# Kernel optimization log

Measured on AMD Instinct MI355X. Metric: run time of the kernel, lower is better.

The kernel has to match this reference:

```python
import jax, jax.numpy as jnp
import numpy as np

INPUT_DIM = 512
HEAD_NUM = 8
ATT_SIZE = 64
EPS = 1e-5


def layer_norm(x, g, b):
    mu = jnp.mean(x, axis=-1, keepdims=True)
    var = jnp.mean(jnp.square(x - mu), axis=-1, keepdims=True)
    return (x - mu) * jax.lax.rsqrt(var + EPS) * g + b


def setup_inputs() -> dict:
    key = jax.random.key(0)
    ks = jax.random.split(key, 10)
    D, H, A = INPUT_DIM, HEAD_NUM, ATT_SIZE
    HA = H * A
    s = lambda fan_in: 1.0 / np.sqrt(fan_in)
    x = jax.random.normal(ks[0], (32, 6, 256, D), dtype=jnp.float32)
    # Linear weights stored as [in, out] so y = x @ W + b (matches torch x @ W.T)
    Wq = jax.random.uniform(ks[1], (D, HA), jnp.float32, -s(D), s(D))
    bq = jnp.zeros((HA,), jnp.float32)
    Wk = jax.random.uniform(ks[2], (D, HA), jnp.float32, -s(D), s(D))
    bk = jnp.zeros((HA,), jnp.float32)
    Wv = jax.random.uniform(ks[3], (D, HA), jnp.float32, -s(D), s(D))
    bv = jnp.zeros((HA,), jnp.float32)
    Wo = jax.random.uniform(ks[4], (HA, D), jnp.float32, -s(HA), s(HA))
    bo = jnp.zeros((D,), jnp.float32)
    g1 = jnp.ones((D,), jnp.float32)
    b1 = jnp.zeros((D,), jnp.float32)
    Wd = jax.random.uniform(ks[5], (2 * D, D), jnp.float32, -s(2 * D), s(2 * D))
    bd = jnp.zeros((D,), jnp.float32)
    g2 = jnp.ones((D,), jnp.float32)
    b2 = jnp.zeros((D,), jnp.float32)
    return dict(x=x, Wq=Wq, bq=bq, Wk=Wk, bk=bk, Wv=Wv, bv=bv,
                Wo=Wo, bo=bo, g1=g1, b1=b1, Wd=Wd, bd=bd, g2=g2, b2=b2)


def reference(x, Wq, bq, Wk, bk, Wv, bv, Wo, bo, g1, b1, Wd, bd, g2, b2):
    B, M, P, D = x.shape
    H, A = HEAD_NUM, ATT_SIZE
    # QKV projections -> [B, M, H, P, A]
    q = (x @ Wq + bq).reshape(B, M, P, H, A).transpose(0, 1, 3, 2, 4)
    k = (x @ Wk + bk).reshape(B, M, P, H, A).transpose(0, 1, 3, 2, 4)
    v = (x @ Wv + bv).reshape(B, M, P, H, A).transpose(0, 1, 3, 2, 4)
    scores = jnp.einsum('bmhqa,bmhka->bmhqk', q, k) / jnp.sqrt(jnp.float32(A))
    attn = jax.nn.softmax(scores, axis=-1)
    z = jnp.einsum('bmhqk,bmhka->bmhqa', attn, v)
    z = z.transpose(0, 1, 3, 2, 4).reshape(B, M, P, H * A)
    z = jax.nn.relu(x + layer_norm(z @ Wo + bo, g1, b1))
    # patch merge (1/2 downsample)
    if P % 2:  # static shape check, fine under jit
        z = jnp.pad(z, ((0, 0), (0, 0), (0, 1), (0, 0)))
    merged = jnp.concatenate([z[:, :, 0::2, :], z[:, :, 1::2, :]], axis=-1)
    out = jax.nn.relu(layer_norm(merged @ Wd + bd, g2, b2))
    return out
```

## Files before the change

### kernel.cpp

```cpp
#include <hip/hip_runtime.h>
#include <hip/hip_bf16.h>
#include <stdint.h>


typedef __hip_bfloat16 bf16;
typedef __attribute__((ext_vector_type(8))) __bf16 bf16v8;
typedef __attribute__((ext_vector_type(4))) float f32x4;
typedef __attribute__((ext_vector_type(8))) short s16x8;
typedef __attribute__((ext_vector_type(4))) short s16x4;

static __device__ __forceinline__ void gl_lds16(const void* src, void* dst) {
  __builtin_amdgcn_global_load_lds((const __attribute__((address_space(1))) void*)src,
                                   (__attribute__((address_space(3))) void*)dst,
                                   16, 0, 0);
}

static __device__ __forceinline__ unsigned short f2bfu(float f) {
  return __builtin_bit_cast(unsigned short, __float2bfloat16(f));
}
static __device__ __forceinline__ float bfu2f(unsigned short u) {
  return __builtin_bit_cast(float, (unsigned int)u << 16);
}

__global__ __launch_bounds__(256) void conv_x_kernel(const float4* __restrict__ x,
                                                     s16x4* __restrict__ xb, int n4) {
  int stride = gridDim.x * 256;
  for (int i = blockIdx.x * 256 + threadIdx.x; i < n4; i += stride) {
    float4 v = x[i];
    s16x4 o;
    o[0] = (short)f2bfu(v.x); o[1] = (short)f2bfu(v.y);
    o[2] = (short)f2bfu(v.z); o[3] = (short)f2bfu(v.w);
    xb[i] = o;
  }
}

__global__ __launch_bounds__(256) void conv_w_kernel(
    const float* __restrict__ Wq, const float* __restrict__ Wk, const float* __restrict__ Wv,
    const float* __restrict__ Wo, const float* __restrict__ Wd,
    const float* __restrict__ bq, const float* __restrict__ bk, const float* __restrict__ bv,
    bf16* __restrict__ wqkv_t, bf16* __restrict__ wo_t, bf16* __restrict__ wd_t,
    float* __restrict__ bqkv) {
  int o = blockIdx.x * 256 + threadIdx.x;
  if (o < 786432) {
    int j = o >> 9, kk = o & 511;
    const float* W = (j < 512) ? Wq : (j < 1024) ? Wk : Wv;
    wqkv_t[o] = __float2bfloat16(W[kk * 512 + (j & 511)]);
  } else if (o < 1048576) {
    int o2 = o - 786432; int j = o2 >> 9, kk = o2 & 511;
    wo_t[o2] = __float2bfloat16(Wo[kk * 512 + j]);
  } else if (o < 1572864) {
    int o3 = o - 1048576; int j = o3 >> 10, kk = o3 & 1023;
    wd_t[o3] = __float2bfloat16(Wd[kk * 512 + j]);
  } else if (o < 1574400) {
    int o4 = o - 1572864;
    const float* b = (o4 < 512) ? bq : (o4 < 1024) ? bk : bv;
    bqkv[o4] = b[o4 & 511];
  }
}

template<int EPI, int AMODE>
__global__ __launch_bounds__(512, 2) void gemm256(
    const bf16* __restrict__ A, const bf16* __restrict__ Bt,
    const float* __restrict__ bias, int K, int nN,
    bf16* __restrict__ oq, bf16* __restrict__ ok, bf16* __restrict__ ovt,
    bf16* __restrict__ obf) {
  __shared__ __align__(16) char smem[131072];
  const int tid = threadIdx.x;
  const int wave = tid >> 6, lane = tid & 63;
  const int wr = wave >> 2, wc = wave & 3;
  const int lane15 = lane & 15, g = lane >> 4;

  const int cpx = gridDim.x >> 3;
  const int lin = (blockIdx.x & 7) * cpx + (blockIdx.x >> 3);
  const int tileM = (lin / nN) * 256, tileN = (lin % nN) * 256;

  const int rT = tid >> 3;
  const int cT = (tid & 7) ^ (rT & 7);
  const int iters = K >> 7;

  auto stage = [&](int tau, int q) {
    char* dst = smem + ((tau & 1) << 16) + ((q >> 1) << 15) + ((q & 1) << 14) + tid * 16;
    int kpos = tau * 64 + cT * 8;
    if (q < 2) {
      int rowA = tileM + ((q & 1) << 7) + rT;
      if (AMODE == 0) {
        const bf16* s0 = A + (size_t)rowA * K + kpos;
        gl_lds16(s0, dst);
        gl_lds16(s0 + (size_t)64 * K, dst + 8192);
      } else {
#pragma unroll
        for (int j = 0; j < 2; ++j) {
          int mr = rowA + j * 64;
          int bm = mr >> 7, pp = mr & 127;
          const bf16* s = A + (size_t)(bm * 256 + pp * 2 + (kpos >> 9)) * 512 + (kpos & 511);
          gl_lds16(s, dst + j * 8192);
        }
      }
    } else {
      int rowB = tileN + ((q & 1) << 7) + rT;
      const bf16* s0 = Bt + (size_t)rowB * K + kpos;
      gl_lds16(s0, dst);
      gl_lds16(s0 + (size_t)64 * K, dst + 8192);
    }
  };

  f32x4 acc[8][4] = {};
  bf16v8 areg[4][2], breg[2][2];

  stage(0, 0); stage(0, 1); stage(0, 2); stage(0, 3);
  stage(1, 0); stage(1, 1);
  asm volatile("s_waitcnt vmcnt(4)" ::: "memory");
  __builtin_amdgcn_s_barrier();

  for (int it = 0; it < iters; ++it) {
    const bool last = (it == iters - 1);
#pragma unroll
    for (int p = 0; p < 8; ++p) {
      const int buf = p >> 2;
      const int mh = (p >> 1) & 1, nh = p & 1;
      char* Ab = smem + (buf << 16);
      char* Bb = Ab + 32768;
      if (nh == 0) {
#pragma unroll
        for (int f = 0; f < 4; ++f) {
          int row = wr * 128 + (mh * 4 + f) * 16 + lane15;
#pragma unroll
          for (int ks = 0; ks < 2; ++ks)
            areg[f][ks] = *(const bf16v8*)(Ab + row * 128 + (((ks * 4 + g) ^ (row & 7)) << 4));
        }
      }
#pragma unroll
      for (int n = 0; n < 2; ++n) {
        int row = wc * 64 + (nh * 2 + n) * 16 + lane15;
#pragma unroll
        for (int ks = 0; ks < 2; ++ks)
          breg[n][ks] = *(const bf16v8*)(Bb + row * 128 + (((ks * 4 + g) ^ (row & 7)) << 4));
      }
      if (p == 0)      { stage(2 * it + 1, 2); stage(2 * it + 1, 3); }
      else if (p == 3) { if (!last) { stage(2 * it + 2, 0); stage(2 * it + 2, 1); } }
      else if (p == 4) { if (!last) { stage(2 * it + 2, 2); stage(2 * it + 2, 3); } }
      else if (p == 7) { if (!last) { stage(2 * it + 3, 0); stage(2 * it + 3, 1); } }
      __builtin_amdgcn_s_setprio(1);
#pragma unroll
      for (int ks = 0; ks < 2; ++ks)
#pragma unroll
        for (int f = 0; f < 4; ++f)
#pragma unroll
          for (int n = 0; n < 2; ++n)
            acc[mh * 4 + f][nh * 2 + n] = __builtin_amdgcn_mfma_f32_16x16x32_bf16(
                areg[f][ks], breg[n][ks], acc[mh * 4 + f][nh * 2 + n], 0, 0, 0);
      __builtin_amdgcn_s_setprio(0);
      if (p == 2 || p == 6) {
        asm volatile("s_waitcnt lgkmcnt(0)" ::: "memory");
        __builtin_amdgcn_s_barrier();
      } else if (p == 3) {
        if (last) { asm volatile("s_waitcnt vmcnt(0) lgkmcnt(0)" ::: "memory"); }
        else      { asm volatile("s_waitcnt vmcnt(4) lgkmcnt(0)" ::: "memory"); }
        __builtin_amdgcn_s_barrier();
      } else if (p == 7) {
        if (last) { asm volatile("s_waitcnt lgkmcnt(0)" ::: "memory"); }
        else      { asm volatile("s_waitcnt vmcnt(4) lgkmcnt(0)" ::: "memory"); }
        __builtin_amdgcn_s_barrier();
      }
    }
  }

  if (EPI == 0 && tileN >= 1024) {
    const int hh = ((tileN - 1024) >> 6) + wc;
    const int bm = tileM >> 8;
    char* slab = smem + wave * 16384;
#pragma unroll
    for (int fm = 0; fm < 8; ++fm) {
#pragma unroll
      for (int fn = 0; fn < 4; ++fn) {
        int col = tileN + wc * 64 + fn * 16 + lane15;
        float bb = bias[col];
        int a = fn * 16 + lane15;
#pragma unroll
        for (int i = 0; i < 4; ++i) {
          int pl = fm * 16 + g * 4 + i;
          *(bf16*)(slab + a * 256 + ((pl * 2) ^ ((a & 7) << 4))) =
              __float2bfloat16(acc[fm][fn][i] + bb);
        }
      }
    }
    asm volatile("" ::: "memory");
    bf16* vdst = ovt + ((size_t)(bm * 8 + hh) << 14) + wr * 128;
#pragma unroll
    for (int r = 0; r < 16; ++r) {
      int a = r * 4 + (lane >> 4);
      int ps = lane & 15;
      s16x8 vv = *(const s16x8*)(slab + a * 256 + ((ps * 16) ^ ((a & 7) << 4)));
      *(s16x8*)(vdst + a * 256 + ps * 8) = vv;
    }
  } else {
    char* slab = smem + wave * 16384;
#pragma unroll
    for (int fm = 0; fm < 8; ++fm) {
#pragma unroll
      for (int fn = 0; fn < 4; ++fn) {
        int col = tileN + wc * 64 + fn * 16 + lane15;
        float bb = bias[col];
        int lb = (fn * 16 + lane15) * 2;
#pragma unroll
        for (int i = 0; i < 4; ++i) {
          int pl = fm * 16 + g * 4 + i;
          *(bf16*)(slab + pl * 128 + (lb ^ ((((pl >> 2) & 3)) << 5))) =
              __float2bfloat16(acc[fm][fn][i] + bb);
        }
      }
    }
    asm volatile("" ::: "memory");
    bf16* dst; int ldc2;
    if (EPI == 0) {
      int cb = tileN + wc * 64;
      int hh = (cb >> 6) & 7;
      bf16* base = (cb < 512) ? oq : ok;
      dst = base + (((size_t)((tileM >> 8) * 8 + hh)) << 14) + wr * 128 * 64;
      ldc2 = 64;
    } else {
      dst = obf + (size_t)(tileM + wr * 128) * 512 + tileN + wc * 64;
      ldc2 = 512;
    }
#pragma unroll
    for (int r = 0; r < 16; ++r) {
      int s = r * 64 + lane;
      int pl = s >> 3, sl = s & 7;
      s16x8 vv = *(const s16x8*)(slab + pl * 128 + ((sl * 16) ^ ((((pl >> 2) & 3)) << 5)));
      *(s16x8*)(dst + (size_t)pl * ldc2 + sl * 8) = vv;
    }
  }
}

__global__ __launch_bounds__(256) void attn_kernel(const bf16* __restrict__ q,
                                                   const bf16* __restrict__ k,
                                                   const bf16* __restrict__ vt,
                                                   bf16* __restrict__ z) {
  __shared__ __align__(16) char smem[81920];
  const int tid = threadIdx.x, wave = tid >> 6, lane = tid & 63;
  const int lane15 = lane & 15, g = lane >> 4;
  const int qc = blockIdx.x, hh = blockIdx.y, bm = blockIdx.z;
  const int bh = bm * 8 + hh;
  const bf16* kbase = k + ((size_t)bh << 14);
  const bf16* vbase = vt + ((size_t)bh << 14);
  const bf16* qbase = q + ((size_t)bh << 14) + (qc * 64 + wave * 16) * 64;

#pragma unroll
  for (int i = 0; i < 8; ++i) {
    int s = i * 256 + tid;
    int kr = s >> 3, ksp = s & 7;
    gl_lds16(kbase + kr * 64 + (ksp ^ (kr & 7)) * 8, smem + s * 16);
    int ar = s >> 5, asp = s & 31;
    gl_lds16(vbase + ar * 256 + (asp ^ (ar & 7)) * 8, smem + 32768 + s * 16);
  }
  bf16v8 qf[2];
#pragma unroll
  for (int kk = 0; kk < 2; ++kk)
    qf[kk] = *(const bf16v8*)(qbase + lane15 * 64 + kk * 32 + g * 8);
  __syncthreads();

  f32x4 sacc[16] = {};
#pragma unroll
  for (int tl = 0; tl < 16; ++tl) {
    int key = tl * 16 + lane15;
    int rb = key * 128, swk = (key & 7) << 4;
#pragma unroll
    for (int kk = 0; kk < 2; ++kk) {
      bf16v8 kf = *(const bf16v8*)(smem + rb + (((kk * 4 + g) * 16) ^ swk));
      sacc[tl] = __builtin_amdgcn_mfma_f32_16x16x32_bf16(qf[kk], kf, sacc[tl], 0, 0, 0);
    }
  }

  float mx[4], sm[4], rcp[4];
#pragma unroll
  for (int i = 0; i < 4; ++i) mx[i] = sacc[0][i];
#pragma unroll
  for (int tl = 1; tl < 16; ++tl)
#pragma unroll
    for (int i = 0; i < 4; ++i) mx[i] = fmaxf(mx[i], sacc[tl][i]);
#pragma unroll
  for (int i = 0; i < 4; ++i) {
    mx[i] = fmaxf(mx[i], __shfl_xor(mx[i], 1));
    mx[i] = fmaxf(mx[i], __shfl_xor(mx[i], 2));
    mx[i] = fmaxf(mx[i], __shfl_xor(mx[i], 4));
    mx[i] = fmaxf(mx[i], __shfl_xor(mx[i], 8));
    sm[i] = 0.f;
  }
#pragma unroll
  for (int tl = 0; tl < 16; ++tl)
#pragma unroll
    for (int i = 0; i < 4; ++i) {
      float e = __expf((sacc[tl][i] - mx[i]) * 0.125f);
      sacc[tl][i] = e; sm[i] += e;
    }
#pragma unroll
  for (int i = 0; i < 4; ++i) {
    sm[i] += __shfl_xor(sm[i], 1);
    sm[i] += __shfl_xor(sm[i], 2);
    sm[i] += __shfl_xor(sm[i], 4);
    sm[i] += __shfl_xor(sm[i], 8);
    rcp[i] = 1.0f / sm[i];
  }

  char* pbase = smem + 65536 + wave * 4096;
  f32x4 oacc[4] = {};
#pragma unroll
  for (int h2 = 0; h2 < 2; ++h2) {
#pragma unroll
    for (int t8 = 0; t8 < 8; ++t8) {
      int tl = h2 * 8 + t8;
#pragma unroll
      for (int i = 0; i < 4; ++i) {
        int r = g * 4 + i;
        int c2 = t8 * 16 + lane15;
        *(bf16*)(pbase + r * 256 + ((c2 * 2) ^ ((r & 7) << 4))) =
            __float2bfloat16(sacc[tl][i] * rcp[i]);
      }
    }
    asm volatile("" ::: "memory");
#pragma unroll
    for (int k2 = 0; k2 < 4; ++k2) {
      int ks = h2 * 4 + k2;
      bf16v8 pf = *(const bf16v8*)(pbase + lane15 * 256 +
                                   ((k2 * 64 + g * 16) ^ ((lane15 & 7) << 4)));
#pragma unroll
      for (int at = 0; at < 4; ++at) {
        int a = at * 16 + lane15;
        bf16v8 vf = *(const bf16v8*)(smem + 32768 + a * 512 +
                                     ((ks * 64 + g * 16) ^ ((a & 7) << 4)));
        oacc[at] = __builtin_amdgcn_mfma_f32_16x16x32_bf16(pf, vf, oacc[at], 0, 0, 0);
      }
    }
    asm volatile("" ::: "memory");
  }

  int trow = bm * 256 + qc * 64 + wave * 16;
#pragma unroll
  for (int at = 0; at < 4; ++at)
#pragma unroll
    for (int i = 0; i < 4; ++i)
      z[(size_t)(trow + g * 4 + i) * 512 + hh * 64 + at * 16 + lane15] =
          __float2bfloat16(oacc[at][i]);
}

static __device__ __forceinline__ float wredsum(float v) {
  v += __shfl_xor(v, 1);  v += __shfl_xor(v, 2);  v += __shfl_xor(v, 4);
  v += __shfl_xor(v, 8);  v += __shfl_xor(v, 16); v += __shfl_xor(v, 32);
  return v;
}

__global__ __launch_bounds__(256) void ln_res_kernel(const bf16* __restrict__ y1,
                                                     const float* __restrict__ x,
                                                     const float* __restrict__ g1,
                                                     const float* __restrict__ b1,
                                                     bf16* __restrict__ z2) {
  const int wave = threadIdx.x >> 6, lane = threadIdx.x & 63;
  const int row = blockIdx.x * 4 + wave;
  const size_t base = (size_t)row * 512 + lane * 8;
  s16x8 yv = *(const s16x8*)(y1 + base);
  float f[8];
#pragma unroll
  for (int j = 0; j < 8; ++j) f[j] = bfu2f((unsigned short)yv[j]);
  float s = 0.f, s2 = 0.f;
#pragma unroll
  for (int j = 0; j < 8; ++j) { s += f[j]; s2 += f[j] * f[j]; }
  s = wredsum(s); s2 = wredsum(s2);
  float mu = s * (1.f / 512.f);
  float var = s2 * (1.f / 512.f) - mu * mu;
  float rs = rsqrtf(var + 1e-5f);
  float4 x0 = *(const float4*)(x + base);
  float4 x1 = *(const float4*)(x + base + 4);
  float xa[8] = {x0.x, x0.y, x0.z, x0.w, x1.x, x1.y, x1.z, x1.w};
  float ga[8], ba[8];
#pragma unroll
  for (int j = 0; j < 8; ++j) { ga[j] = g1[lane * 8 + j]; ba[j] = b1[lane * 8 + j]; }
  s16x8 ov;
#pragma unroll
  for (int j = 0; j < 8; ++j) {
    float v = xa[j] + (f[j] - mu) * rs * ga[j] + ba[j];
    ov[j] = (short)f2bfu(fmaxf(v, 0.f));
  }
  *(s16x8*)(z2 + base) = ov;
}

__global__ __launch_bounds__(256) void ln_out_kernel(const bf16* __restrict__ y2,
                                                     const float* __restrict__ g2,
                                                     const float* __restrict__ b2,
                                                     float* __restrict__ out) {
  const int wave = threadIdx.x >> 6, lane = threadIdx.x & 63;
  const int row = blockIdx.x * 4 + wave;
  const size_t base = (size_t)row * 512 + lane * 8;
  s16x8 yv = *(const s16x8*)(y2 + base);
  float f[8];
#pragma unroll
  for (int j = 0; j < 8; ++j) f[j] = bfu2f((unsigned short)yv[j]);
  float s = 0.f, s2 = 0.f;
#pragma unroll
  for (int j = 0; j < 8; ++j) { s += f[j]; s2 += f[j] * f[j]; }
  s = wredsum(s); s2 = wredsum(s2);
  float mu = s * (1.f / 512.f);
  float var = s2 * (1.f / 512.f) - mu * mu;
  float rs = rsqrtf(var + 1e-5f);
  float o[8];
#pragma unroll
  for (int j = 0; j < 8; ++j)
    o[j] = fmaxf((f[j] - mu) * rs * g2[lane * 8 + j] + b2[lane * 8 + j], 0.f);
  float4 w0 = {o[0], o[1], o[2], o[3]};
  float4 w1 = {o[4], o[5], o[6], o[7]};
  *(float4*)(out + base) = w0;
  *(float4*)(out + base + 4) = w1;
}

extern "C" void kernel_launch(void* const* d_in, const int* in_sizes, int n_in,
                              void* d_out, int out_size, void* d_ws, size_t ws_size,
                              hipStream_t stream) {
  const float* x  = (const float*)d_in[0];
  const float* Wq = (const float*)d_in[1];
  const float* bq = (const float*)d_in[2];
  const float* Wk = (const float*)d_in[3];
  const float* bk = (const float*)d_in[4];
  const float* Wv = (const float*)d_in[5];
  const float* bv = (const float*)d_in[6];
  const float* Wo = (const float*)d_in[7];
  const float* bo = (const float*)d_in[8];
  const float* g1 = (const float*)d_in[9];
  const float* b1 = (const float*)d_in[10];
  const float* Wd = (const float*)d_in[11];
  const float* bd = (const float*)d_in[12];
  const float* g2 = (const float*)d_in[13];
  const float* b2 = (const float*)d_in[14];

  char* ws = (char*)d_ws;
  const size_t SEG = 50331648;
  bf16*  xb   = (bf16*)(ws);
  bf16*  qb   = (bf16*)(ws + SEG);
  bf16*  kb   = (bf16*)(ws + 2 * SEG);
  bf16*  vtb  = (bf16*)(ws + 3 * SEG);
  bf16*  wqkv = (bf16*)(ws + 4 * SEG);
  bf16*  wot  = (bf16*)(ws + 4 * SEG + 1572864);
  bf16*  wdt  = (bf16*)(ws + 4 * SEG + 2097152);
  float* bqkv = (float*)(ws + 4 * SEG + 3145728);
  bf16*  zb   = xb;
  bf16*  y1   = qb;
  bf16*  z2   = kb;
  bf16*  y2   = vtb;

  conv_x_kernel<<<4096, 256, 0, stream>>>((const float4*)x, (s16x4*)xb, 25165824 / 4);
  conv_w_kernel<<<6150, 256, 0, stream>>>(Wq, Wk, Wv, Wo, Wd, bq, bk, bv,
                                          wqkv, wot, wdt, bqkv);
  gemm256<0, 0><<<1152, 512, 0, stream>>>(xb, wqkv, bqkv, 512, 6,
                                          qb, kb, vtb, nullptr);
  attn_kernel<<<dim3(4, 8, 192), 256, 0, stream>>>(qb, kb, vtb, zb);
  gemm256<1, 0><<<384, 512, 0, stream>>>(zb, wot, bo, 512, 2,
                                         nullptr, nullptr, nullptr, y1);
  ln_res_kernel<<<12288, 256, 0, stream>>>(y1, x, g1, b1, z2);
  gemm256<1, 1><<<192, 512, 0, stream>>>(z2, wdt, bd, 1024, 2,
                                         nullptr, nullptr, nullptr, y2);
  ln_out_kernel<<<6144, 256, 0, stream>>>(y2, g2, b2, (float*)d_out);
}
```

Baseline: 332.5 us.

## Shrink GEMM tiles from 256x256 to 128x128 with 4-wave blocks

Replaces the 256x256, 512-thread GEMM with a 128x128, 256-thread version that uses half the LDS, and adapts the staging, fragment loads and epilogues to the new tile. All three GEMM launches now use 4x more blocks, which improves wave fill across the CUs, especially for the small out-projection and downsample GEMMs that had only 384 and 192 blocks. The trade-off is lower arithmetic intensity per tile and more global/L2 traffic for operand reloads. It also caches B fragments across phases to avoid re-reading LDS.

```diff
diff --git a/kernel.cpp b/kernel.cpp
--- a/kernel.cpp
+++ b/kernel.cpp
@@ -59,53 +59,51 @@
 }
 
 template<int EPI, int AMODE>
-__global__ __launch_bounds__(512, 2) void gemm256(
+__global__ __launch_bounds__(256, 2) void gemm128(
     const bf16* __restrict__ A, const bf16* __restrict__ Bt,
     const float* __restrict__ bias, int K, int nN,
     bf16* __restrict__ oq, bf16* __restrict__ ok, bf16* __restrict__ ovt,
     bf16* __restrict__ obf) {
-  __shared__ __align__(16) char smem[131072];
+  __shared__ __align__(16) char smem[65536];
   const int tid = threadIdx.x;
   const int wave = tid >> 6, lane = tid & 63;
-  const int wr = wave >> 2, wc = wave & 3;
+  const int wr = wave >> 1, wc = wave & 1;
   const int lane15 = lane & 15, g = lane >> 4;
 
   const int cpx = gridDim.x >> 3;
   const int lin = (blockIdx.x & 7) * cpx + (blockIdx.x >> 3);
-  const int tileM = (lin / nN) * 256, tileN = (lin % nN) * 256;
-
-  const int rT = tid >> 3;
-  const int cT = (tid & 7) ^ (rT & 7);
+  const int tileM = (lin / nN) * 128, tileN = (lin % nN) * 128;
+
   const int iters = K >> 7;
 
   auto stage = [&](int tau, int q) {
-    char* dst = smem + ((tau & 1) << 16) + ((q >> 1) << 15) + ((q & 1) << 14) + tid * 16;
-    int kpos = tau * 64 + cT * 8;
-    if (q < 2) {
-      int rowA = tileM + ((q & 1) << 7) + rT;
-      if (AMODE == 0) {
-        const bf16* s0 = A + (size_t)rowA * K + kpos;
-        gl_lds16(s0, dst);
-        gl_lds16(s0 + (size_t)64 * K, dst + 8192);
+    char* dstb = smem + ((tau & 1) << 15) + ((q >> 1) << 14) + ((q & 1) << 13);
+#pragma unroll
+    for (int u = 0; u < 2; ++u) {
+      int slot = u * 256 + tid;
+      int r = slot >> 3;
+      int c = (slot & 7) ^ (r & 7);
+      int kpos = tau * 64 + c * 8;
+      if (q < 2) {
+        int mr = tileM + ((q & 1) << 6) + r;
+        const bf16* s;
+        if (AMODE == 0) {
+          s = A + (size_t)mr * K + kpos;
+        } else {
+          int bm = mr >> 7, pp = mr & 127;
+          s = A + (size_t)(bm * 256 + pp * 2 + (kpos >> 9)) * 512 + (kpos & 511);
+        }
+        gl_lds16(s, dstb + slot * 16);
       } else {
-#pragma unroll
-        for (int j = 0; j < 2; ++j) {
-          int mr = rowA + j * 64;
-          int bm = mr >> 7, pp = mr & 127;
-          const bf16* s = A + (size_t)(bm * 256 + pp * 2 + (kpos >> 9)) * 512 + (kpos & 511);
-          gl_lds16(s, dst + j * 8192);
-        }
-      }
-    } else {
-      int rowB = tileN + ((q & 1) << 7) + rT;
-      const bf16* s0 = Bt + (size_t)rowB * K + kpos;
-      gl_lds16(s0, dst);
-      gl_lds16(s0 + (size_t)64 * K, dst + 8192);
+        int nr = tileN + ((q & 1) << 6) + r;
+        gl_lds16(Bt + (size_t)nr * K + kpos, dstb + slot * 16);
+      }
     }
   };
 
-  f32x4 acc[8][4] = {};
-  bf16v8 areg[4][2], breg[2][2];
+  f32x4 acc[4][4] = {};
+  bf16v8 areg[2][2], breg[2][2][2];
+  const int swl = (lane15 & 7);
 
   stage(0, 0); stage(0, 1); stage(0, 2); stage(0, 3);
   stage(1, 0); stage(1, 1);
@@ -118,23 +116,25 @@
     for (int p = 0; p < 8; ++p) {
       const int buf = p >> 2;
       const int mh = (p >> 1) & 1, nh = p & 1;
-      char* Ab = smem + (buf << 16);
-      char* Bb = Ab + 32768;
+      char* Ab = smem + (buf << 15);
+      char* Bb = Ab + 16384;
       if (nh == 0) {
 #pragma unroll
-        for (int f = 0; f < 4; ++f) {
-          int row = wr * 128 + (mh * 4 + f) * 16 + lane15;
+        for (int f = 0; f < 2; ++f) {
+          int row = wr * 64 + mh * 32 + f * 16 + lane15;
 #pragma unroll
           for (int ks = 0; ks < 2; ++ks)
-            areg[f][ks] = *(const bf16v8*)(Ab + row * 128 + (((ks * 4 + g) ^ (row & 7)) << 4));
+            areg[f][ks] = *(const bf16v8*)(Ab + row * 128 + (((ks * 4 + g) ^ swl) << 4));
         }
       }
-#pragma unroll
-      for (int n = 0; n < 2; ++n) {
-        int row = wc * 64 + (nh * 2 + n) * 16 + lane15;
-#pragma unroll
-        for (int ks = 0; ks < 2; ++ks)
-          breg[n][ks] = *(const bf16v8*)(Bb + row * 128 + (((ks * 4 + g) ^ (row & 7)) << 4));
+      if ((p & 3) <= 1) {
+#pragma unroll
+        for (int n = 0; n < 2; ++n) {
+          int row = wc * 64 + nh * 32 + n * 16 + lane15;
+#pragma unroll
+          for (int ks = 0; ks < 2; ++ks)
+            breg[nh][n][ks] = *(const bf16v8*)(Bb + row * 128 + (((ks * 4 + g) ^ swl) << 4));
+        }
       }
       if (p == 0)      { stage(2 * it + 1, 2); stage(2 * it + 1, 3); }
       else if (p == 3) { if (!last) { stage(2 * it + 2, 0); stage(2 * it + 2, 1); } }
@@ -144,11 +144,11 @@
 #pragma unroll
       for (int ks = 0; ks < 2; ++ks)
 #pragma unroll
-        for (int f = 0; f < 4; ++f)
+        for (int f = 0; f < 2; ++f)
 #pragma unroll
           for (int n = 0; n < 2; ++n)
-            acc[mh * 4 + f][nh * 2 + n] = __builtin_amdgcn_mfma_f32_16x16x32_bf16(
-                areg[f][ks], breg[n][ks], acc[mh * 4 + f][nh * 2 + n], 0, 0, 0);
+            acc[mh * 2 + f][nh * 2 + n] = __builtin_amdgcn_mfma_f32_16x16x32_bf16(
+                areg[f][ks], breg[nh][n][ks], acc[mh * 2 + f][nh * 2 + n], 0, 0, 0);
       __builtin_amdgcn_s_setprio(0);
       if (p == 2 || p == 6) {
         asm volatile("s_waitcnt lgkmcnt(0)" ::: "memory");
@@ -165,38 +165,39 @@
     }
   }
 
+  const int rowstart = tileM + wr * 64;
   if (EPI == 0 && tileN >= 1024) {
-    const int hh = ((tileN - 1024) >> 6) + wc;
-    const int bm = tileM >> 8;
-    char* slab = smem + wave * 16384;
-#pragma unroll
-    for (int fm = 0; fm < 8; ++fm) {
+    const int cb = tileN + wc * 64;
+    const int hh = (cb - 1024) >> 6;
+    const int bmq = rowstart >> 8, p0off = rowstart & 255;
+    char* slab = smem + wave * 8192;
+#pragma unroll
+    for (int fm = 0; fm < 4; ++fm) {
 #pragma unroll
       for (int fn = 0; fn < 4; ++fn) {
-        int col = tileN + wc * 64 + fn * 16 + lane15;
-        float bb = bias[col];
+        float bb = bias[cb + fn * 16 + lane15];
         int a = fn * 16 + lane15;
 #pragma unroll
         for (int i = 0; i < 4; ++i) {
           int pl = fm * 16 + g * 4 + i;
-          *(bf16*)(slab + a * 256 + ((pl * 2) ^ ((a & 7) << 4))) =
+          *(bf16*)(slab + a * 128 + ((pl * 2) ^ ((a & 7) << 4))) =
               __float2bfloat16(acc[fm][fn][i] + bb);
         }
       }
     }
     asm volatile("" ::: "memory");
-    bf16* vdst = ovt + ((size_t)(bm * 8 + hh) << 14) + wr * 128;
-#pragma unroll
-    for (int r = 0; r < 16; ++r) {
-      int a = r * 4 + (lane >> 4);
-      int ps = lane & 15;
-      s16x8 vv = *(const s16x8*)(slab + a * 256 + ((ps * 16) ^ ((a & 7) << 4)));
+    bf16* vdst = ovt + ((size_t)(bmq * 8 + hh) << 14) + p0off;
+#pragma unroll
+    for (int r = 0; r < 8; ++r) {
+      int a = r * 8 + (lane >> 3);
+      int ps = lane & 7;
+      s16x8 vv = *(const s16x8*)(slab + a * 128 + ((ps * 16) ^ ((a & 7) << 4)));
       *(s16x8*)(vdst + a * 256 + ps * 8) = vv;
     }
   } else {
-    char* slab = smem + wave * 16384;
-#pragma unroll
-    for (int fm = 0; fm < 8; ++fm) {
+    char* slab = smem + wave * 8192;
+#pragma unroll
+    for (int fm = 0; fm < 4; ++fm) {
 #pragma unroll
       for (int fn = 0; fn < 4; ++fn) {
         int col = tileN + wc * 64 + fn * 16 + lane15;
@@ -216,14 +217,14 @@
       int cb = tileN + wc * 64;
       int hh = (cb >> 6) & 7;
       bf16* base = (cb < 512) ? oq : ok;
-      dst = base + (((size_t)((tileM >> 8) * 8 + hh)) << 14) + wr * 128 * 64;
+      dst = base + (((size_t)((rowstart >> 8) * 8 + hh)) << 14) + (rowstart & 255) * 64;
       ldc2 = 64;
     } else {
-      dst = obf + (size_t)(tileM + wr * 128) * 512 + tileN + wc * 64;
+      dst = obf + (size_t)rowstart * 512 + tileN + wc * 64;
       ldc2 = 512;
     }
 #pragma unroll
-    for (int r = 0; r < 16; ++r) {
+    for (int r = 0; r < 8; ++r) {
       int s = r * 64 + lane;
       int pl = s >> 3, sl = s & 7;
       s16x8 vv = *(const s16x8*)(slab + pl * 128 + ((sl * 16) ^ ((((pl >> 2) & 3)) << 5)));
@@ -448,13 +449,13 @@
   conv_x_kernel<<<4096, 256, 0, stream>>>((const float4*)x, (s16x4*)xb, 25165824 / 4);
   conv_w_kernel<<<6150, 256, 0, stream>>>(Wq, Wk, Wv, Wo, Wd, bq, bk, bv,
                                           wqkv, wot, wdt, bqkv);
-  gemm256<0, 0><<<1152, 512, 0, stream>>>(xb, wqkv, bqkv, 512, 6,
+  gemm128<0, 0><<<4608, 256, 0, stream>>>(xb, wqkv, bqkv, 512, 12,
                                           qb, kb, vtb, nullptr);
   attn_kernel<<<dim3(4, 8, 192), 256, 0, stream>>>(qb, kb, vtb, zb);
-  gemm256<1, 0><<<384, 512, 0, stream>>>(zb, wot, bo, 512, 2,
-                                         nullptr, nullptr, nullptr, y1);
+  gemm128<1, 0><<<1536, 256, 0, stream>>>(zb, wot, bo, 512, 4,
+                                          nullptr, nullptr, nullptr, y1);
   ln_res_kernel<<<12288, 256, 0, stream>>>(y1, x, g1, b1, z2);
-  gemm256<1, 1><<<192, 512, 0, stream>>>(z2, wdt, bd, 1024, 2,
+  gemm128<1, 1><<<768, 256, 0, stream>>>(z2, wdt, bd, 1024, 4,
                                          nullptr, nullptr, nullptr, y2);
   ln_out_kernel<<<6144, 256, 0, stream>>>(y2, g2, b2, (float*)d_out);
 }
```

New measurement: 317.3 us. 4.6% less time.
